# Optimization experiments

Hardware: AMD Instinct MI355X
Metric: run time of the kernel (lower is better)

The kernel has to match this reference:

```python
import jax, jax.numpy as jnp
import numpy as np

B, H, L, P = 16, 256, 8192, 64  # batch, d_input, seq_len, d_state


def setup_inputs() -> dict:
    key = jax.random.key(0)
    k1, k2, k3, k4, k5, k6 = jax.random.split(key, 6)
    u = jax.random.normal(k1, (B, H, L), dtype=jnp.float32)
    # diagonal SSM poles on an annulus inside the unit disk (stable discrete dynamics)
    radius = jax.random.uniform(k2, (P,), minval=0.5, maxval=0.99)
    theta = jax.random.uniform(k3, (P,), minval=0.0, maxval=2.0 * np.pi)
    A_re = (radius * jnp.cos(theta)).astype(jnp.float32)
    A_im = (radius * jnp.sin(theta)).astype(jnp.float32)
    # combined input/output mixing W = C*B, complex (H, P)
    BC_re = (jax.random.normal(k4, (H, P)) / np.sqrt(P)).astype(jnp.float32)
    BC_im = (jax.random.normal(k5, (H, P)) / np.sqrt(P)).astype(jnp.float32)
    # D skip vector: uniform_ring(min_radius=0.0, max_radius=1.0, field='real')
    D = jax.random.uniform(k6, (H,), minval=0.0, maxval=1.0, dtype=jnp.float32)
    return {"u": u, "A_re": A_re, "A_im": A_im, "BC_re": BC_re, "BC_im": BC_im, "D": D}


def reference(u, A_re, A_im, BC_re, BC_im, D):
    # Vandermonde kernel: k[h, l] = sum_p BC[h, p] * A[p]**l, computed stably via exp(l*log A)
    A = jax.lax.complex(A_re, A_im)                      # (P,)
    logA = jnp.log(A)                                    # (P,) complex
    ell = jnp.arange(L, dtype=jnp.float32)               # (L,)
    V = jnp.exp(logA[:, None] * ell[None, :])            # (P, L) complex Vandermonde
    BC = jax.lax.complex(BC_re, BC_im)                   # (H, P)
    k = jnp.einsum('hp,pl->hl', BC, V)                   # (H, L) complex kernel
    # circular FFT convolution (same-length fft/ifft as the torch code)
    u_s = jnp.fft.fft(u, axis=-1)                        # (B, H, L) complex
    k_s = jnp.fft.fft(k, axis=-1)                        # (H, L) complex
    y = jnp.fft.ifft(u_s * k_s[None, :, :], axis=-1).real
    y = y + D[None, :, None] * u                         # D*u skip
    return jnp.tanh(y)                                   # activation (dropout=0 -> identity)
```

## Files before the change

### kernel.cpp

```cpp
#include <hip/hip_runtime.h>
#include <cmath>


typedef _Float16 half8 __attribute__((ext_vector_type(8)));
typedef _Float16 half4v __attribute__((ext_vector_type(4)));
typedef _Float16 half2v __attribute__((ext_vector_type(2)));
typedef float floatx16 __attribute__((ext_vector_type(16)));

#define NC 64
#define CM 128
#define A2_BYTES ((size_t)256 * 128 * 256 * 2)
#define W_BYTES  ((size_t)128 * 128 * 2)
#define AM_OFF   (A2_BYTES + W_BYTES)

#define SWH(r, c) ((((r) << 7)) | ((c) ^ (((r) & 15) << 3)))

__device__ __forceinline__ float fast_tanh(float x) {
    float e2 = __expf(2.0f * x);
    return 1.0f - 2.0f / (e2 + 1.0f);
}

__global__ void fftconv_prep(const float* __restrict__ A_re, const float* __restrict__ A_im,
                             const float* __restrict__ BC_re, const float* __restrict__ BC_im,
                             const float* __restrict__ Dv, char* __restrict__ ws) {
    __shared__ float rr[64], th[64], br[64], bi[64];
    __shared__ float kk[CM];
    const int h = blockIdx.x, tid = threadIdx.x;
    if (tid < 64) {
        float x = A_re[tid], y = A_im[tid];
        rr[tid] = log2f(sqrtf(x * x + y * y));
        th[tid] = atan2f(y, x);
        br[tid] = BC_re[h * 64 + tid];
        bi[tid] = BC_im[h * 64 + tid];
    }
    __syncthreads();
    if (tid < CM) {
        float d = (float)tid, s = 0.f;
        for (int p = 0; p < 64; ++p) {
            float mag = exp2f(d * rr[p]);
            float ang = d * th[p];
            s += mag * (br[p] * cosf(ang) - bi[p] * sinf(ang));
        }
        kk[tid] = s;
    }
    __syncthreads();
    _Float16* A2 = (_Float16*)ws + (size_t)h * 128 * 256;
    const float Dh = Dv[h];
    for (int idx = tid; idx < 128 * 128; idx += 256) {
        int r = idx >> 7, pc = idx & 127, p = pc & 63;
        float e = (float)(r + 1);
        float mag = exp2f(e * rr[p]);
        float ang = e * th[p];
        float cr = mag * cosf(ang), ci = mag * sinf(ang);
        float val = (pc < 64) ? (br[p] * cr - bi[p] * ci) : -(br[p] * ci + bi[p] * cr);
        int cn = ((pc & 63) << 1) | (pc >> 6);
        A2[r * 256 + cn] = (_Float16)val;
    }
    for (int idx = tid; idx < 128 * 128; idx += 256) {
        int r = idx >> 7, j = idx & 127;
        float v = (j <= r) ? kk[r - j] : 0.f;
        if (j == r) v += Dh;
        A2[r * 256 + CM + j] = (_Float16)v;
    }
    if (h == 0) {
        _Float16* W = (_Float16*)(ws + A2_BYTES);
        for (int idx = tid; idx < 128 * 128; idx += 256) {
            int pc = idx >> 7, j = idx & 127, p = pc & 63;
            float e = (float)(127 - j);
            float mag = exp2f(e * rr[p]);
            float ang = e * th[p];
            float v = (pc < 64) ? mag * cosf(ang) : mag * sinf(ang);
            int rn = ((pc & 63) << 1) | (pc >> 6);
            W[rn * 128 + j] = (_Float16)v;
        }
        if (tid < 64) {
            float mag = exp2f(128.f * rr[tid]);
            float ang = 128.f * th[tid];
            float* aM = (float*)(ws + AM_OFF);
            aM[tid] = mag * cosf(ang);
            aM[64 + tid] = mag * sinf(ang);
        }
    }
}

__global__ __launch_bounds__(256, 4)
void fftconv_main(const float* __restrict__ u, const char* __restrict__ ws,
                  float* __restrict__ out) {
    __shared__ __align__(16) _Float16 u16[NC * CM];
    __shared__ __align__(16) _Float16 S16[NC * CM];

    const int tid = threadIdx.x;
    const int lane = tid & 63;
    const int wv = tid >> 6;
    const int h = blockIdx.x >> 4;
    const int bb = blockIdx.x & 15;
    const float* ub = u + ((size_t)bb * 256 + h) * 8192;
    float* yb = out + ((size_t)bb * 256 + h) * 8192;

    const int mrow = (wv << 5) + (lane & 31);
    const int kh = (lane >> 5) << 3;
    const int ncol = lane & 31;

    const _Float16* Wg = (const _Float16*)(ws + A2_BYTES) + (size_t)mrow * CM + kh;
    const _Float16* Ag = (const _Float16*)ws + ((size_t)h * CM + mrow) * 256 + kh;

    float4 uv[8];
#pragma unroll
    for (int i = 0; i < 8; ++i) uv[i] = ((const float4*)ub)[i * 256 + tid];
    half8 wf[8];
#pragma unroll
    for (int s = 0; s < 8; ++s) wf[s] = *(const half8*)(Wg + (s << 4));

#pragma unroll
    for (int i = 0; i < 8; ++i) {
        int e4 = i * 256 + tid;
        int c = e4 >> 5, j = (e4 << 2) & 127;
        half4v hv = { (_Float16)uv[i].x, (_Float16)uv[i].y,
                      (_Float16)uv[i].z, (_Float16)uv[i].w };
        *(half4v*)&u16[SWH(c, j)] = hv;
    }
    half8 tf[8];
#pragma unroll
    for (int s = 0; s < 8; ++s) tf[s] = *(const half8*)(Ag + CM + (s << 4));
    __syncthreads();

    {
        floatx16 acc0 = {}; floatx16 acc1 = {};
#pragma unroll
        for (int s = 0; s < 8; ++s) {
            int k0 = (s << 4) + kh;
            half8 b0 = *(const half8*)&u16[SWH(ncol, k0)];
            half8 b1 = *(const half8*)&u16[SWH(ncol + 32, k0)];
            acc0 = __builtin_amdgcn_mfma_f32_32x32x16_f16(wf[s], b0, acc0, 0, 0, 0);
            acc1 = __builtin_amdgcn_mfma_f32_32x32x16_f16(wf[s], b1, acc1, 0, 0, 0);
        }
        const int pc0 = (wv << 5) + ((lane >> 5) << 2);
#pragma unroll
        for (int g = 0; g < 4; ++g) {
            half4v h0 = { (_Float16)acc0[4 * g + 0], (_Float16)acc0[4 * g + 1],
                          (_Float16)acc0[4 * g + 2], (_Float16)acc0[4 * g + 3] };
            *(half4v*)&S16[SWH(ncol, pc0 + 8 * g)] = h0;
            half4v h1 = { (_Float16)acc1[4 * g + 0], (_Float16)acc1[4 * g + 1],
                          (_Float16)acc1[4 * g + 2], (_Float16)acc1[4 * g + 3] };
            *(half4v*)&S16[SWH(ncol + 32, pc0 + 8 * g)] = h1;
        }
    }
    __syncthreads();

    floatx16 y0 = {}; floatx16 y1 = {};
    float er[16], ei[16];
    {
        const float* aM = (const float*)(ws + AM_OFF);
        const float amr = aM[lane], ami = aM[64 + lane];
        const int cbase = wv << 4;
        float sr = 0.f, si = 0.f, pr = 1.f, pi = 0.f;
#pragma unroll
        for (int d = 0; d < 8; ++d) {
            int cc = (cbase - 1 - d) & 63;
            half2v xv = *(const half2v*)&S16[SWH(cc, lane << 1)];
            float xr = (float)xv.x, xi = (float)xv.y;
            sr = fmaf(pr, xr, fmaf(-pi, xi, sr));
            si = fmaf(pr, xi, fmaf(pi, xr, si));
            float npr = pr * amr - pi * ami;
            float npi = pr * ami + pi * amr;
            pr = npr; pi = npi;
        }
        er[0] = sr; ei[0] = si;
#pragma unroll
        for (int s = 0; s < 8; ++s) {
            int k0 = (s << 4) + kh;
            half8 b0 = *(const half8*)&u16[SWH(ncol, k0)];
            half8 b1 = *(const half8*)&u16[SWH(ncol + 32, k0)];
            y0 = __builtin_amdgcn_mfma_f32_32x32x16_f16(tf[s], b0, y0, 0, 0, 0);
            y1 = __builtin_amdgcn_mfma_f32_32x32x16_f16(tf[s], b1, y1, 0, 0, 0);
#pragma unroll
            for (int t = 1; t <= 2; ++t) {
                int i = 2 * s + t;
                if (i < 16) {
                    half2v xv = *(const half2v*)&S16[SWH(cbase + i - 1, lane << 1)];
                    float xr = (float)xv.x, xi = (float)xv.y;
                    er[i] = fmaf(amr, er[i - 1], fmaf(-ami, ei[i - 1], xr));
                    ei[i] = fmaf(amr, ei[i - 1], fmaf(ami, er[i - 1], xi));
                }
            }
        }
    }
    __syncthreads();

    half8 gf[8];
#pragma unroll
    for (int s = 0; s < 8; ++s) gf[s] = *(const half8*)(Ag + (s << 4));

#pragma unroll
    for (int i = 0; i < 16; ++i) {
        int c = (wv << 4) + i;
        half2v ev = { (_Float16)er[i], (_Float16)ei[i] };
        *(half2v*)&S16[SWH(c, lane << 1)] = ev;
    }
    __syncthreads();

    {
#pragma unroll
        for (int s = 0; s < 8; ++s) {
            int k0 = (s << 4) + kh;
            half8 b0 = *(const half8*)&S16[SWH(ncol, k0)];
            half8 b1 = *(const half8*)&S16[SWH(ncol + 32, k0)];
            y0 = __builtin_amdgcn_mfma_f32_32x32x16_f16(gf[s], b0, y0, 0, 0, 0);
            y1 = __builtin_amdgcn_mfma_f32_32x32x16_f16(gf[s], b1, y1, 0, 0, 0);
        }
        const int r0 = (wv << 5) + ((lane >> 5) << 2);
#pragma unroll
        for (int g = 0; g < 4; ++g) {
            float4 o0;
            o0.x = fast_tanh(y0[4 * g + 0]); o0.y = fast_tanh(y0[4 * g + 1]);
            o0.z = fast_tanh(y0[4 * g + 2]); o0.w = fast_tanh(y0[4 * g + 3]);
            *(float4*)(yb + (size_t)ncol * CM + r0 + 8 * g) = o0;
            float4 o1;
            o1.x = fast_tanh(y1[4 * g + 0]); o1.y = fast_tanh(y1[4 * g + 1]);
            o1.z = fast_tanh(y1[4 * g + 2]); o1.w = fast_tanh(y1[4 * g + 3]);
            *(float4*)(yb + (size_t)(ncol + 32) * CM + r0 + 8 * g) = o1;
        }
    }
}

extern "C" void kernel_launch(void* const* d_in, const int* in_sizes, int n_in,
                              void* d_out, int out_size, void* d_ws, size_t ws_size,
                              hipStream_t stream) {
    const float* u     = (const float*)d_in[0];
    const float* A_re  = (const float*)d_in[1];
    const float* A_im  = (const float*)d_in[2];
    const float* BC_re = (const float*)d_in[3];
    const float* BC_im = (const float*)d_in[4];
    const float* Dv    = (const float*)d_in[5];
    float* out = (float*)d_out;
    char* ws = (char*)d_ws;

    hipLaunchKernelGGL(fftconv_prep, dim3(256), dim3(256), 0, stream,
                       A_re, A_im, BC_re, BC_im, Dv, ws);
    hipLaunchKernelGGL(fftconv_main, dim3(4096), dim3(256), 0, stream,
                       u, ws, out);
}
```

Baseline: 342.1 us.

## Process two batch rows per block, reusing weight fragments and prefetching next input

```diff
diff --git a/kernel.cpp b/kernel.cpp
--- a/kernel.cpp
+++ b/kernel.cpp
@@ -83,19 +83,17 @@
     }
 }
 
-__global__ __launch_bounds__(256, 4)
+__global__ __launch_bounds__(256, 3)
 void fftconv_main(const float* __restrict__ u, const char* __restrict__ ws,
                   float* __restrict__ out) {
-    __shared__ __align__(16) _Float16 u16[NC * CM];
+    __shared__ __align__(16) _Float16 u16[2][NC * CM];
     __shared__ __align__(16) _Float16 S16[NC * CM];
 
     const int tid = threadIdx.x;
     const int lane = tid & 63;
     const int wv = tid >> 6;
-    const int h = blockIdx.x >> 4;
-    const int bb = blockIdx.x & 15;
-    const float* ub = u + ((size_t)bb * 256 + h) * 8192;
-    float* yb = out + ((size_t)bb * 256 + h) * 8192;
+    const int h = blockIdx.x & 255;
+    const int bbg = blockIdx.x >> 8;
 
     const int mrow = (wv << 5) + (lane & 31);
     const int kh = (lane >> 5) << 3;
@@ -104,122 +102,143 @@
     const _Float16* Wg = (const _Float16*)(ws + A2_BYTES) + (size_t)mrow * CM + kh;
     const _Float16* Ag = (const _Float16*)ws + ((size_t)h * CM + mrow) * 256 + kh;
 
-    float4 uv[8];
-#pragma unroll
-    for (int i = 0; i < 8; ++i) uv[i] = ((const float4*)ub)[i * 256 + tid];
-    half8 wf[8];
+    const float* ub0 = u + ((size_t)((bbg * 2 + 0) * 256) + h) * 8192;
+    const float* ub1 = u + ((size_t)((bbg * 2 + 1) * 256) + h) * 8192;
+
+    float4 uvA[8];
+#pragma unroll
+    for (int i = 0; i < 8; ++i) uvA[i] = ((const float4*)ub0)[i * 256 + tid];
+    half8 wf[8], tf[8];
 #pragma unroll
     for (int s = 0; s < 8; ++s) wf[s] = *(const half8*)(Wg + (s << 4));
+#pragma unroll
+    for (int s = 0; s < 8; ++s) tf[s] = *(const half8*)(Ag + CM + (s << 4));
 
 #pragma unroll
     for (int i = 0; i < 8; ++i) {
         int e4 = i * 256 + tid;
         int c = e4 >> 5, j = (e4 << 2) & 127;
-        half4v hv = { (_Float16)uv[i].x, (_Float16)uv[i].y,
-                      (_Float16)uv[i].z, (_Float16)uv[i].w };
-        *(half4v*)&u16[SWH(c, j)] = hv;
-    }
-    half8 tf[8];
-#pragma unroll
-    for (int s = 0; s < 8; ++s) tf[s] = *(const half8*)(Ag + CM + (s << 4));
+        half4v hv = { (_Float16)uvA[i].x, (_Float16)uvA[i].y,
+                      (_Float16)uvA[i].z, (_Float16)uvA[i].w };
+        *(half4v*)&u16[0][SWH(c, j)] = hv;
+    }
+    float4 uvB[8];
+#pragma unroll
+    for (int i = 0; i < 8; ++i) uvB[i] = ((const float4*)ub1)[i * 256 + tid];
+    half8 gf[8];
     __syncthreads();
 
-    {
-        floatx16 acc0 = {}; floatx16 acc1 = {};
-#pragma unroll
-        for (int s = 0; s < 8; ++s) {
-            int k0 = (s << 4) + kh;
-            half8 b0 = *(const half8*)&u16[SWH(ncol, k0)];
-            half8 b1 = *(const half8*)&u16[SWH(ncol + 32, k0)];
-            acc0 = __builtin_amdgcn_mfma_f32_32x32x16_f16(wf[s], b0, acc0, 0, 0, 0);
-            acc1 = __builtin_amdgcn_mfma_f32_32x32x16_f16(wf[s], b1, acc1, 0, 0, 0);
-        }
-        const int pc0 = (wv << 5) + ((lane >> 5) << 2);
-#pragma unroll
-        for (int g = 0; g < 4; ++g) {
-            half4v h0 = { (_Float16)acc0[4 * g + 0], (_Float16)acc0[4 * g + 1],
-                          (_Float16)acc0[4 * g + 2], (_Float16)acc0[4 * g + 3] };
-            *(half4v*)&S16[SWH(ncol, pc0 + 8 * g)] = h0;
-            half4v h1 = { (_Float16)acc1[4 * g + 0], (_Float16)acc1[4 * g + 1],
-                          (_Float16)acc1[4 * g + 2], (_Float16)acc1[4 * g + 3] };
-            *(half4v*)&S16[SWH(ncol + 32, pc0 + 8 * g)] = h1;
-        }
-    }
-    __syncthreads();
-
-    floatx16 y0 = {}; floatx16 y1 = {};
-    float er[16], ei[16];
-    {
-        const float* aM = (const float*)(ws + AM_OFF);
-        const float amr = aM[lane], ami = aM[64 + lane];
-        const int cbase = wv << 4;
-        float sr = 0.f, si = 0.f, pr = 1.f, pi = 0.f;
-#pragma unroll
-        for (int d = 0; d < 8; ++d) {
-            int cc = (cbase - 1 - d) & 63;
-            half2v xv = *(const half2v*)&S16[SWH(cc, lane << 1)];
-            float xr = (float)xv.x, xi = (float)xv.y;
-            sr = fmaf(pr, xr, fmaf(-pi, xi, sr));
-            si = fmaf(pr, xi, fmaf(pi, xr, si));
-            float npr = pr * amr - pi * ami;
-            float npi = pr * ami + pi * amr;
-            pr = npr; pi = npi;
-        }
-        er[0] = sr; ei[0] = si;
-#pragma unroll
-        for (int s = 0; s < 8; ++s) {
-            int k0 = (s << 4) + kh;
-            half8 b0 = *(const half8*)&u16[SWH(ncol, k0)];
-            half8 b1 = *(const half8*)&u16[SWH(ncol + 32, k0)];
-            y0 = __builtin_amdgcn_mfma_f32_32x32x16_f16(tf[s], b0, y0, 0, 0, 0);
-            y1 = __builtin_amdgcn_mfma_f32_32x32x16_f16(tf[s], b1, y1, 0, 0, 0);
-#pragma unroll
-            for (int t = 1; t <= 2; ++t) {
-                int i = 2 * s + t;
-                if (i < 16) {
-                    half2v xv = *(const half2v*)&S16[SWH(cbase + i - 1, lane << 1)];
-                    float xr = (float)xv.x, xi = (float)xv.y;
-                    er[i] = fmaf(amr, er[i - 1], fmaf(-ami, ei[i - 1], xr));
-                    ei[i] = fmaf(amr, ei[i - 1], fmaf(ami, er[i - 1], xi));
-                }
-            }
-        }
-    }
-    __syncthreads();
-
-    half8 gf[8];
-#pragma unroll
-    for (int s = 0; s < 8; ++s) gf[s] = *(const half8*)(Ag + (s << 4));
-
-#pragma unroll
-    for (int i = 0; i < 16; ++i) {
-        int c = (wv << 4) + i;
-        half2v ev = { (_Float16)er[i], (_Float16)ei[i] };
-        *(half2v*)&S16[SWH(c, lane << 1)] = ev;
-    }
-    __syncthreads();
-
-    {
-#pragma unroll
-        for (int s = 0; s < 8; ++s) {
-            int k0 = (s << 4) + kh;
-            half8 b0 = *(const half8*)&S16[SWH(ncol, k0)];
-            half8 b1 = *(const half8*)&S16[SWH(ncol + 32, k0)];
-            y0 = __builtin_amdgcn_mfma_f32_32x32x16_f16(gf[s], b0, y0, 0, 0, 0);
-            y1 = __builtin_amdgcn_mfma_f32_32x32x16_f16(gf[s], b1, y1, 0, 0, 0);
-        }
-        const int r0 = (wv << 5) + ((lane >> 5) << 2);
-#pragma unroll
-        for (int g = 0; g < 4; ++g) {
-            float4 o0;
-            o0.x = fast_tanh(y0[4 * g + 0]); o0.y = fast_tanh(y0[4 * g + 1]);
-            o0.z = fast_tanh(y0[4 * g + 2]); o0.w = fast_tanh(y0[4 * g + 3]);
-            *(float4*)(yb + (size_t)ncol * CM + r0 + 8 * g) = o0;
-            float4 o1;
-            o1.x = fast_tanh(y1[4 * g + 0]); o1.y = fast_tanh(y1[4 * g + 1]);
-            o1.z = fast_tanh(y1[4 * g + 2]); o1.w = fast_tanh(y1[4 * g + 3]);
-            *(float4*)(yb + (size_t)(ncol + 32) * CM + r0 + 8 * g) = o1;
-        }
+#pragma unroll
+    for (int sq = 0; sq < 2; ++sq) {
+        const _Float16* ub16 = u16[sq];
+
+        {
+            floatx16 a0 = {}; floatx16 a1 = {};
+#pragma unroll
+            for (int s = 0; s < 8; ++s) {
+                int k0 = (s << 4) + kh;
+                half8 b0 = *(const half8*)&ub16[SWH(ncol, k0)];
+                half8 b1 = *(const half8*)&ub16[SWH(ncol + 32, k0)];
+                a0 = __builtin_amdgcn_mfma_f32_32x32x16_f16(wf[s], b0, a0, 0, 0, 0);
+                a1 = __builtin_amdgcn_mfma_f32_32x32x16_f16(wf[s], b1, a1, 0, 0, 0);
+            }
+            const int pc0 = (wv << 5) + ((lane >> 5) << 2);
+#pragma unroll
+            for (int g = 0; g < 4; ++g) {
+                half4v h0 = { (_Float16)a0[4 * g + 0], (_Float16)a0[4 * g + 1],
+                              (_Float16)a0[4 * g + 2], (_Float16)a0[4 * g + 3] };
+                *(half4v*)&S16[SWH(ncol, pc0 + 8 * g)] = h0;
+                half4v h1 = { (_Float16)a1[4 * g + 0], (_Float16)a1[4 * g + 1],
+                              (_Float16)a1[4 * g + 2], (_Float16)a1[4 * g + 3] };
+                *(half4v*)&S16[SWH(ncol + 32, pc0 + 8 * g)] = h1;
+            }
+        }
+        if (sq == 0) {
+#pragma unroll
+            for (int i = 0; i < 8; ++i) {
+                int e4 = i * 256 + tid;
+                int c = e4 >> 5, j = (e4 << 2) & 127;
+                half4v hv = { (_Float16)uvB[i].x, (_Float16)uvB[i].y,
+                              (_Float16)uvB[i].z, (_Float16)uvB[i].w };
+                *(half4v*)&u16[1][SWH(c, j)] = hv;
+            }
+        }
+        __syncthreads();
+
+        float er[16], ei[16];
+        {
+            const float* aM = (const float*)(ws + AM_OFF);
+            const float amr = aM[lane], ami = aM[64 + lane];
+            const int cbase = wv << 4;
+            float sr = 0.f, si = 0.f, pr = 1.f, pi = 0.f;
+#pragma unroll
+            for (int d = 0; d < 8; ++d) {
+                int cc = (cbase - 1 - d) & 63;
+                half2v xv = *(const half2v*)&S16[SWH(cc, lane << 1)];
+                float xr = (float)xv.x, xi = (float)xv.y;
+                sr = fmaf(pr, xr, fmaf(-pi, xi, sr));
+                si = fmaf(pr, xi, fmaf(pi, xr, si));
+                float npr = pr * amr - pi * ami;
+                float npi = pr * ami + pi * amr;
+                pr = npr; pi = npi;
+            }
+            er[0] = sr; ei[0] = si;
+#pragma unroll
+            for (int i = 1; i < 16; ++i) {
+                half2v xv = *(const half2v*)&S16[SWH(cbase + i - 1, lane << 1)];
+                float xr = (float)xv.x, xi = (float)xv.y;
+                er[i] = fmaf(amr, er[i - 1], fmaf(-ami, ei[i - 1], xr));
+                ei[i] = fmaf(amr, ei[i - 1], fmaf(ami, er[i - 1], xi));
+            }
+        }
+        __syncthreads();
+
+        if (sq == 0) {
+#pragma unroll
+            for (int s = 0; s < 8; ++s) gf[s] = *(const half8*)(Ag + (s << 4));
+        }
+
+#pragma unroll
+        for (int i = 0; i < 16; ++i) {
+            int c = (wv << 4) + i;
+            half2v ev = { (_Float16)er[i], (_Float16)ei[i] };
+            *(half2v*)&S16[SWH(c, lane << 1)] = ev;
+        }
+        __syncthreads();
+
+        {
+            floatx16 y0 = {}; floatx16 y1 = {};
+#pragma unroll
+            for (int s = 0; s < 8; ++s) {
+                int k0 = (s << 4) + kh;
+                half8 b0 = *(const half8*)&S16[SWH(ncol, k0)];
+                half8 b1 = *(const half8*)&S16[SWH(ncol + 32, k0)];
+                y0 = __builtin_amdgcn_mfma_f32_32x32x16_f16(gf[s], b0, y0, 0, 0, 0);
+                y1 = __builtin_amdgcn_mfma_f32_32x32x16_f16(gf[s], b1, y1, 0, 0, 0);
+            }
+#pragma unroll
+            for (int s = 0; s < 8; ++s) {
+                int k0 = (s << 4) + kh;
+                half8 b0 = *(const half8*)&ub16[SWH(ncol, k0)];
+                half8 b1 = *(const half8*)&ub16[SWH(ncol + 32, k0)];
+                y0 = __builtin_amdgcn_mfma_f32_32x32x16_f16(tf[s], b0, y0, 0, 0, 0);
+                y1 = __builtin_amdgcn_mfma_f32_32x32x16_f16(tf[s], b1, y1, 0, 0, 0);
+            }
+            float* yb = out + ((size_t)((bbg * 2 + sq) * 256) + h) * 8192;
+            const int r0 = (wv << 5) + ((lane >> 5) << 2);
+#pragma unroll
+            for (int g = 0; g < 4; ++g) {
+                float4 o0;
+                o0.x = fast_tanh(y0[4 * g + 0]); o0.y = fast_tanh(y0[4 * g + 1]);
+                o0.z = fast_tanh(y0[4 * g + 2]); o0.w = fast_tanh(y0[4 * g + 3]);
+                *(float4*)(yb + (size_t)ncol * CM + r0 + 8 * g) = o0;
+                float4 o1;
+                o1.x = fast_tanh(y1[4 * g + 0]); o1.y = fast_tanh(y1[4 * g + 1]);
+                o1.z = fast_tanh(y1[4 * g + 2]); o1.w = fast_tanh(y1[4 * g + 3]);
+                *(float4*)(yb + (size_t)(ncol + 32) * CM + r0 + 8 * g) = o1;
+            }
+        }
+        if (sq == 0) __syncthreads();
     }
 }
 
@@ -237,6 +256,6 @@
 
     hipLaunchKernelGGL(fftconv_prep, dim3(256), dim3(256), 0, stream,
                        A_re, A_im, BC_re, BC_im, Dv, ws);
-    hipLaunchKernelGGL(fftconv_main, dim3(4096), dim3(256), 0, stream,
+    hipLaunchKernelGGL(fftconv_main, dim3(2048), dim3(256), 0, stream,
                        u, ws, out);
 }
```

New measurement: 350.9 us. 1.03x slower.

## Split each sequence into two half-segments per block with history chunks

Applied to the files above, without the earlier changes.

```diff
diff --git a/kernel.cpp b/kernel.cpp
--- a/kernel.cpp
+++ b/kernel.cpp
@@ -9,6 +9,8 @@
 
 #define NC 64
 #define CM 128
+#define CSTG 40
+#define HIST 8
 #define A2_BYTES ((size_t)256 * 128 * 256 * 2)
 #define W_BYTES  ((size_t)128 * 128 * 2)
 #define AM_OFF   (A2_BYTES + W_BYTES)
@@ -86,14 +88,16 @@
 __global__ __launch_bounds__(256, 4)
 void fftconv_main(const float* __restrict__ u, const char* __restrict__ ws,
                   float* __restrict__ out) {
-    __shared__ __align__(16) _Float16 u16[NC * CM];
-    __shared__ __align__(16) _Float16 S16[NC * CM];
+    __shared__ __align__(16) _Float16 u16[CSTG * CM];
+    __shared__ __align__(16) _Float16 S16[CSTG * CM];
 
     const int tid = threadIdx.x;
     const int lane = tid & 63;
     const int wv = tid >> 6;
-    const int h = blockIdx.x >> 4;
-    const int bb = blockIdx.x & 15;
+    const int h = blockIdx.x & 255;
+    const int seg = blockIdx.x >> 8;
+    const int bb = seg >> 1;
+    const int c0 = (seg & 1) << 5;
     const float* ub = u + ((size_t)bb * 256 + h) * 8192;
     float* yb = out + ((size_t)bb * 256 + h) * 8192;
 
@@ -104,20 +108,25 @@
     const _Float16* Wg = (const _Float16*)(ws + A2_BYTES) + (size_t)mrow * CM + kh;
     const _Float16* Ag = (const _Float16*)ws + ((size_t)h * CM + mrow) * 256 + kh;
 
-    float4 uv[8];
-#pragma unroll
-    for (int i = 0; i < 8; ++i) uv[i] = ((const float4*)ub)[i * 256 + tid];
+    float4 uv[5];
+#pragma unroll
+    for (int i = 0; i < 5; ++i) {
+        int e4 = i * 256 + tid;
+        int lc = e4 >> 5, q = e4 & 31;
+        int gc = (c0 - HIST + lc) & 63;
+        uv[i] = ((const float4*)ub)[gc * 32 + q];
+    }
     half8 wf[8];
 #pragma unroll
     for (int s = 0; s < 8; ++s) wf[s] = *(const half8*)(Wg + (s << 4));
 
 #pragma unroll
-    for (int i = 0; i < 8; ++i) {
+    for (int i = 0; i < 5; ++i) {
         int e4 = i * 256 + tid;
-        int c = e4 >> 5, j = (e4 << 2) & 127;
+        int lc = e4 >> 5, j = (e4 & 31) << 2;
         half4v hv = { (_Float16)uv[i].x, (_Float16)uv[i].y,
                       (_Float16)uv[i].z, (_Float16)uv[i].w };
-        *(half4v*)&u16[SWH(c, j)] = hv;
+        *(half4v*)&u16[SWH(lc, j)] = hv;
     }
     half8 tf[8];
 #pragma unroll
@@ -125,39 +134,37 @@
     __syncthreads();
 
     {
-        floatx16 acc0 = {}; floatx16 acc1 = {};
+        floatx16 a0 = {}; floatx16 a1 = {};
 #pragma unroll
         for (int s = 0; s < 8; ++s) {
             int k0 = (s << 4) + kh;
             half8 b0 = *(const half8*)&u16[SWH(ncol, k0)];
-            half8 b1 = *(const half8*)&u16[SWH(ncol + 32, k0)];
-            acc0 = __builtin_amdgcn_mfma_f32_32x32x16_f16(wf[s], b0, acc0, 0, 0, 0);
-            acc1 = __builtin_amdgcn_mfma_f32_32x32x16_f16(wf[s], b1, acc1, 0, 0, 0);
+            half8 b1 = *(const half8*)&u16[SWH(ncol + HIST, k0)];
+            a0 = __builtin_amdgcn_mfma_f32_32x32x16_f16(wf[s], b0, a0, 0, 0, 0);
+            a1 = __builtin_amdgcn_mfma_f32_32x32x16_f16(wf[s], b1, a1, 0, 0, 0);
         }
         const int pc0 = (wv << 5) + ((lane >> 5) << 2);
 #pragma unroll
         for (int g = 0; g < 4; ++g) {
-            half4v h0 = { (_Float16)acc0[4 * g + 0], (_Float16)acc0[4 * g + 1],
-                          (_Float16)acc0[4 * g + 2], (_Float16)acc0[4 * g + 3] };
+            half4v h0 = { (_Float16)a0[4 * g + 0], (_Float16)a0[4 * g + 1],
+                          (_Float16)a0[4 * g + 2], (_Float16)a0[4 * g + 3] };
             *(half4v*)&S16[SWH(ncol, pc0 + 8 * g)] = h0;
-            half4v h1 = { (_Float16)acc1[4 * g + 0], (_Float16)acc1[4 * g + 1],
-                          (_Float16)acc1[4 * g + 2], (_Float16)acc1[4 * g + 3] };
-            *(half4v*)&S16[SWH(ncol + 32, pc0 + 8 * g)] = h1;
-        }
-    }
-    __syncthreads();
-
-    floatx16 y0 = {}; floatx16 y1 = {};
-    float er[16], ei[16];
+            half4v h1 = { (_Float16)a1[4 * g + 0], (_Float16)a1[4 * g + 1],
+                          (_Float16)a1[4 * g + 2], (_Float16)a1[4 * g + 3] };
+            *(half4v*)&S16[SWH(ncol + HIST, pc0 + 8 * g)] = h1;
+        }
+    }
+    __syncthreads();
+
+    float er[8], ei[8];
     {
         const float* aM = (const float*)(ws + AM_OFF);
         const float amr = aM[lane], ami = aM[64 + lane];
-        const int cbase = wv << 4;
+        const int cb = HIST + (wv << 3);
         float sr = 0.f, si = 0.f, pr = 1.f, pi = 0.f;
 #pragma unroll
         for (int d = 0; d < 8; ++d) {
-            int cc = (cbase - 1 - d) & 63;
-            half2v xv = *(const half2v*)&S16[SWH(cc, lane << 1)];
+            half2v xv = *(const half2v*)&S16[SWH(cb - 1 - d, lane << 1)];
             float xr = (float)xv.x, xi = (float)xv.y;
             sr = fmaf(pr, xr, fmaf(-pi, xi, sr));
             si = fmaf(pr, xi, fmaf(pi, xr, si));
@@ -167,46 +174,40 @@
         }
         er[0] = sr; ei[0] = si;
 #pragma unroll
+        for (int i = 1; i < 8; ++i) {
+            half2v xv = *(const half2v*)&S16[SWH(cb + i - 1, lane << 1)];
+            float xr = (float)xv.x, xi = (float)xv.y;
+            er[i] = fmaf(amr, er[i - 1], fmaf(-ami, ei[i - 1], xr));
+            ei[i] = fmaf(amr, ei[i - 1], fmaf(ami, er[i - 1], xi));
+        }
+    }
+    __syncthreads();
+
+    half8 gf[8];
+#pragma unroll
+    for (int s = 0; s < 8; ++s) gf[s] = *(const half8*)(Ag + (s << 4));
+
+#pragma unroll
+    for (int i = 0; i < 8; ++i) {
+        int lc = HIST + (wv << 3) + i;
+        half2v ev = { (_Float16)er[i], (_Float16)ei[i] };
+        *(half2v*)&S16[SWH(lc, lane << 1)] = ev;
+    }
+    __syncthreads();
+
+    {
+        floatx16 y0 = {};
+#pragma unroll
         for (int s = 0; s < 8; ++s) {
             int k0 = (s << 4) + kh;
-            half8 b0 = *(const half8*)&u16[SWH(ncol, k0)];
-            half8 b1 = *(const half8*)&u16[SWH(ncol + 32, k0)];
-            y0 = __builtin_amdgcn_mfma_f32_32x32x16_f16(tf[s], b0, y0, 0, 0, 0);
-            y1 = __builtin_amdgcn_mfma_f32_32x32x16_f16(tf[s], b1, y1, 0, 0, 0);
-#pragma unroll
-            for (int t = 1; t <= 2; ++t) {
-                int i = 2 * s + t;
-                if (i < 16) {
-                    half2v xv = *(const half2v*)&S16[SWH(cbase + i - 1, lane << 1)];
-                    float xr = (float)xv.x, xi = (float)xv.y;
-                    er[i] = fmaf(amr, er[i - 1], fmaf(-ami, ei[i - 1], xr));
-                    ei[i] = fmaf(amr, ei[i - 1], fmaf(ami, er[i - 1], xi));
-                }
-            }
-        }
-    }
-    __syncthreads();
-
-    half8 gf[8];
-#pragma unroll
-    for (int s = 0; s < 8; ++s) gf[s] = *(const half8*)(Ag + (s << 4));
-
-#pragma unroll
-    for (int i = 0; i < 16; ++i) {
-        int c = (wv << 4) + i;
-        half2v ev = { (_Float16)er[i], (_Float16)ei[i] };
-        *(half2v*)&S16[SWH(c, lane << 1)] = ev;
-    }
-    __syncthreads();
-
-    {
+            half8 b0 = *(const half8*)&S16[SWH(ncol + HIST, k0)];
+            y0 = __builtin_amdgcn_mfma_f32_32x32x16_f16(gf[s], b0, y0, 0, 0, 0);
+        }
 #pragma unroll
         for (int s = 0; s < 8; ++s) {
             int k0 = (s << 4) + kh;
-            half8 b0 = *(const half8*)&S16[SWH(ncol, k0)];
-            half8 b1 = *(const half8*)&S16[SWH(ncol + 32, k0)];
-            y0 = __builtin_amdgcn_mfma_f32_32x32x16_f16(gf[s], b0, y0, 0, 0, 0);
-            y1 = __builtin_amdgcn_mfma_f32_32x32x16_f16(gf[s], b1, y1, 0, 0, 0);
+            half8 b0 = *(const half8*)&u16[SWH(ncol + HIST, k0)];
+            y0 = __builtin_amdgcn_mfma_f32_32x32x16_f16(tf[s], b0, y0, 0, 0, 0);
         }
         const int r0 = (wv << 5) + ((lane >> 5) << 2);
 #pragma unroll
@@ -214,11 +215,7 @@
             float4 o0;
             o0.x = fast_tanh(y0[4 * g + 0]); o0.y = fast_tanh(y0[4 * g + 1]);
             o0.z = fast_tanh(y0[4 * g + 2]); o0.w = fast_tanh(y0[4 * g + 3]);
-            *(float4*)(yb + (size_t)ncol * CM + r0 + 8 * g) = o0;
-            float4 o1;
-            o1.x = fast_tanh(y1[4 * g + 0]); o1.y = fast_tanh(y1[4 * g + 1]);
-            o1.z = fast_tanh(y1[4 * g + 2]); o1.w = fast_tanh(y1[4 * g + 3]);
-            *(float4*)(yb + (size_t)(ncol + 32) * CM + r0 + 8 * g) = o1;
+            *(float4*)(yb + (size_t)(c0 + ncol) * CM + r0 + 8 * g) = o0;
         }
     }
 }
@@ -237,6 +234,6 @@
 
     hipLaunchKernelGGL(fftconv_prep, dim3(256), dim3(256), 0, stream,
                        A_re, A_im, BC_re, BC_im, Dv, ws);
-    hipLaunchKernelGGL(fftconv_main, dim3(4096), dim3(256), 0, stream,
+    hipLaunchKernelGGL(fftconv_main, dim3(8192), dim3(256), 0, stream,
                        u, ws, out);
 }
```

New measurement: 369.1 us. +7.9%, slower.
